# Kernel tuning notes

Measured on AMD Instinct MI355X. Metric: run time of the kernel, lower is better.

The kernel has to match this reference:

```python
import jax, jax.numpy as jnp
import numpy as np

B = 16      # graphs
NPG = 1024  # nodes per graph (equal-sized, contiguous)
N = B * NPG
K = 12      # knn neighbors
DM = 128    # d_model
DH = 256    # d_hidden = 2*d_model
L = 3       # num_layers
DI = 2 * DM + 4  # msg mlp input dim


def _mlp2(x, W1, b1, W2, b2):
    return jax.nn.silu(x @ W1 + b1) @ W2 + b2


def setup_inputs() -> dict:
    key = jax.random.key(0)
    ks = list(jax.random.split(key, 16))
    def nrm(k, shape, fan):
        return jax.random.normal(k, shape, jnp.float32) / np.float32(np.sqrt(fan))
    return dict(
        x=jax.random.normal(ks[0], (N, 3), jnp.float32),
        batch=(jnp.arange(N) // NPG).astype(jnp.int32),
        in_W1=nrm(ks[1], (3, DM), 3), in_b1=jnp.zeros((DM,), jnp.float32),
        in_W2=nrm(ks[2], (DM, DM), DM), in_b2=jnp.zeros((DM,), jnp.float32),
        msg_W1=nrm(ks[3], (L, DI, DH), DI), msg_b1=jnp.zeros((L, DH), jnp.float32),
        msg_W2=nrm(ks[4], (L, DH, DM), DH), msg_b2=jnp.zeros((L, DM), jnp.float32),
        upd_W1=nrm(ks[5], (L, 2 * DM, DH), 2 * DM), upd_b1=jnp.zeros((L, DH), jnp.float32),
        upd_W2=nrm(ks[6], (L, DH, DM), DH), upd_b2=jnp.zeros((L, DM), jnp.float32),
        norm_w=jnp.ones((L, DM), jnp.float32), norm_b=jnp.zeros((L, DM), jnp.float32),
        norm_ms=jnp.ones((L, DM), jnp.float32),
        gate_W1=nrm(ks[7], (DM, DM), DM), gate_b1=jnp.zeros((DM,), jnp.float32),
        gate_W2=nrm(ks[8], (DM, 1), DM), gate_b2=jnp.zeros((1,), jnp.float32),
        head_W1=nrm(ks[9], (DM, DM), DM), head_b1=jnp.zeros((DM,), jnp.float32),
        head_W2=nrm(ks[10], (DM, 1), DM), head_b2=jnp.zeros((1,), jnp.float32),
    )


def _knn_edges(pos):
    # pos: [N,2]; graphs are contiguous blocks of NPG nodes -> blocked knn
    p3 = pos.reshape(B, NPG, 2)
    d2 = jnp.sum((p3[:, :, None, :] - p3[:, None, :, :]) ** 2, axis=-1)  # [B,n,n]
    d2 = jnp.where(jnp.eye(NPG, dtype=bool)[None], jnp.inf, d2)          # no self loops
    idx = jax.lax.top_k(-d2, K)[1]  # [B,n,K] nearest neighbors (sources)
    offs = (jnp.arange(B) * NPG)[:, None, None]
    src = (idx + offs).reshape(-1)
    dst = jnp.broadcast_to(jnp.arange(N).reshape(B, NPG, 1), (B, NPG, K)).reshape(-1)
    return src, dst


def _graph_norm(h, batch, cnt, w, b, ms):
    # PyG GraphNorm: out = w * (h - ms*mean) / sqrt(var + eps) + b, per-graph stats
    mean = jax.ops.segment_sum(h, batch, B) / cnt
    out = h - mean[batch] * ms
    var = jax.ops.segment_sum(out ** 2, batch, B) / cnt
    return w * out / jnp.sqrt(var + 1e-5)[batch] + b


def _forward(x, batch, in_W1, in_b1, in_W2, in_b2, msg_W1, msg_b1, msg_W2, msg_b2,
             upd_W1, upd_b1, upd_W2, upd_b2, norm_w, norm_b, norm_ms,
             gate_W1, gate_b1, gate_W2, gate_b2, head_W1, head_b1, head_W2, head_b2):
    pos = x[:, 1:3]
    src, dst = _knn_edges(pos)
    # edge_attr = [dx, dy, dist, ds]
    dp = pos[src] - pos[dst]
    dist = jnp.sqrt(jnp.sum(dp ** 2, axis=-1, keepdims=True) + 1e-12)
    ds = x[src, 0:1] - x[dst, 0:1]
    ea = jnp.concatenate([dp, dist, ds], axis=-1)  # [E,4]

    h = _mlp2(x, in_W1, in_b1, in_W2, in_b2)       # [N,DM]
    cnt = jax.ops.segment_sum(jnp.ones((N,), h.dtype), batch, B)[:, None]

    for i in range(L):
        m_in = jnp.concatenate([h[dst], h[src], ea], axis=-1)       # [E,2*DM+4]
        m = _mlp2(m_in, msg_W1[i], msg_b1[i], msg_W2[i], msg_b2[i])  # [E,DM]
        agg = jax.ops.segment_sum(m, dst, N)                         # scatter_add
        dh = _mlp2(jnp.concatenate([h, agg], axis=-1),
                   upd_W1[i], upd_b1[i], upd_W2[i], upd_b2[i])
        h = h + dh  # dropout is identity at inference
        h = _graph_norm(h, batch, cnt, norm_w[i], norm_b[i], norm_ms[i])

    # gated attention pool: segment softmax over gate logits
    gl = (jnp.tanh(h @ gate_W1 + gate_b1) @ gate_W2 + gate_b2)[:, 0]  # [N]
    gmax = jax.ops.segment_max(gl, batch, B)
    e = jnp.exp(gl - gmax[batch])
    a = e / jax.ops.segment_sum(e, batch, B)[batch]
    pooled = jax.ops.segment_sum(h * a[:, None], batch, B)            # [B,DM]

    return _mlp2(pooled, head_W1, head_b1, head_W2, head_b2)[:, 0]    # [B]


def reference(x, batch, in_W1, in_b1, in_W2, in_b2, msg_W1, msg_b1, msg_W2, msg_b2,
              upd_W1, upd_b1, upd_W2, upd_b2, norm_w, norm_b, norm_ms,
              gate_W1, gate_b1, gate_W2, gate_b2, head_W1, head_b1, head_W2, head_b2):
    return _forward(x, batch, in_W1, in_b1, in_W2, in_b2, msg_W1, msg_b1, msg_W2, msg_b2,
                    upd_W1, upd_b1, upd_W2, upd_b2, norm_w, norm_b, norm_ms,
                    gate_W1, gate_b1, gate_W2, gate_b2, head_W1, head_b1, head_W2, head_b2)
```

## Files before the change

kernel.cpp:

```cpp
#include <hip/hip_runtime.h>
#include <math.h>

#define NPTS 16384
#define BGR 16
#define NPGR 1024
#define KNN 12
#define DM 128
#define DH 256
#define NL 3
#define EDG (NPTS*KNN)

typedef unsigned short u16;
typedef unsigned int u32;
typedef __attribute__((ext_vector_type(8))) short short8;
typedef __attribute__((ext_vector_type(4))) float floatx4;

__device__ __forceinline__ float silu_f(float x) {
    return x / (1.0f + __expf(-x));
}
__device__ __forceinline__ u16 f2bf(float f) {
    union { float f; u32 u; } v; v.f = f;
    u32 r = v.u + 0x7fffu + ((v.u >> 16) & 1u);
    return (u16)(r >> 16);
}
__device__ __forceinline__ float bf2f(u16 b) {
    union { u32 u; float f; } v; v.u = ((u32)b) << 16;
    return v.f;
}

#define KPPB 16
#define PSTR 209
__global__ __launch_bounds__(256) void knn_kernel(const float* __restrict__ x,
                                                  int* __restrict__ srcb,
                                                  float* __restrict__ ea) {
#pragma clang fp contract(off)
    __shared__ float px[NPGR], py[NPGR], s0[NPGR];
    __shared__ float sdf[KPPB * PSTR];
    __shared__ int   sif[KPPB * PSTR];
    __shared__ int   sel[KPPB][KNN];
    int t = threadIdx.x;
    int g   = blockIdx.x / (NPGR / KPPB);
    int blk = blockIdx.x % (NPGR / KPPB);
    int base = g * NPGR;
    for (int j = t; j < NPGR; j += 256) {
        const float* xp = x + (size_t)(base + j) * 3;
        s0[j] = xp[0]; px[j] = xp[1]; py[j] = xp[2];
    }
    __syncthreads();
    int r  = t & 15;
    int pt = t >> 4;
    int il = blk * KPPB + pt;
    float xi = px[il], yi = py[il];
    float nd[KNN]; int ni[KNN];
#pragma unroll
    for (int k = 0; k < KNN; ++k) { nd[k] = 3.4e38f; ni[k] = 0x7fffffff; }
    int j0 = r * 64;
    for (int jj = 0; jj < 64; ++jj) {
        int j = j0 + jj;
        if (j == il) continue;
        float dx = px[j] - xi;
        float dy = py[j] - yi;
        float dx2 = dx * dx;
        float dy2 = dy * dy;
        float d2 = dx2 + dy2;
        if (d2 < nd[KNN-1]) {
            float cd = d2; int ci = j;
#pragma unroll
            for (int k = 0; k < KNN; ++k) {
                bool sw = cd < nd[k];
                float tdv = sw ? nd[k] : cd;
                nd[k] = sw ? cd : nd[k];
                cd = tdv;
                int tiv = sw ? ni[k] : ci;
                ni[k] = sw ? ci : ni[k];
                ci = tiv;
            }
        }
    }
#pragma unroll
    for (int k = 0; k < KNN; ++k) {
        sdf[pt * PSTR + r * 13 + k] = nd[k];
        sif[pt * PSTR + r * 13 + k] = ni[k];
    }
    __syncthreads();
    if (r == 0) {
        int head[16];
#pragma unroll
        for (int q = 0; q < 16; ++q) head[q] = 0;
#pragma unroll
        for (int k = 0; k < KNN; ++k) {
            float bd = 3.4e38f; int bi = 0x7fffffff; int bq = 0;
#pragma unroll
            for (int q = 0; q < 16; ++q) {
                int hq = head[q];
                float d = (hq < KNN) ? sdf[pt * PSTR + q * 13 + hq] : 3.4e38f;
                int  ix = (hq < KNN) ? sif[pt * PSTR + q * 13 + hq] : 0x7fffffff;
                if (d < bd || (d == bd && ix < bi)) { bd = d; bi = ix; bq = q; }
            }
            head[bq]++;
            sel[pt][k] = bi;
        }
    }
    __syncthreads();
    if (r < KNN) {
        int k = r;
        int j = sel[pt][k];
        size_t e = (size_t)(base + il) * KNN + k;
        srcb[e] = base + j;
        float x0i = s0[il];
        float dpx = px[j] - xi, dpy = py[j] - yi;
        float a = dpx * dpx;
        float b = dpy * dpy;
        float dist = sqrtf(a + b + 1e-12f);
        float dsv = s0[j] - x0i;
        *(float4*)(ea + e * 4) = make_float4(dpx, dpy, dist, dsv);
    }
}

__global__ __launch_bounds__(128) void in_mlp_kernel(const float* __restrict__ x,
    const float* __restrict__ W1, const float* __restrict__ b1,
    const float* __restrict__ W2, const float* __restrict__ b2,
    float* __restrict__ h) {
    __shared__ float hid[8][DM];
    __shared__ float xl[8][3];
    int t = threadIdx.x;
    int nb = blockIdx.x * 8;
    if (t < 24) xl[t / 3][t % 3] = x[(size_t)nb * 3 + t];
    __syncthreads();
    float w0 = W1[t], w1 = W1[DM + t], w2 = W1[2 * DM + t], bb = b1[t];
#pragma unroll
    for (int gi = 0; gi < 8; ++gi) {
        float v = xl[gi][0] * w0 + xl[gi][1] * w1 + xl[gi][2] * w2 + bb;
        hid[gi][t] = silu_f(v);
    }
    __syncthreads();
    float acc[8];
    float b2v = b2[t];
#pragma unroll
    for (int gi = 0; gi < 8; ++gi) acc[gi] = b2v;
    for (int k = 0; k < DM; ++k) {
        float w = W2[k * DM + t];
#pragma unroll
        for (int gi = 0; gi < 8; ++gi) acc[gi] += hid[gi][k] * w;
    }
#pragma unroll
    for (int gi = 0; gi < 8; ++gi) h[(size_t)(nb + gi) * DM + t] = acc[gi];
}

#define MBM 64
#define MBN 128
#define MBK 32
#define MLDA 40

__global__ __launch_bounds__(256) void mgemm_kernel(
    const float* __restrict__ A0, int k0, int lda0,
    const float* __restrict__ A1, int lda1,
    const u16* __restrict__ Wh, const u16* __restrict__ Wl, int K,
    const float* __restrict__ bias, int biasN,
    const float* __restrict__ resid, int ldres,
    float* __restrict__ out, int ldout,
    int act)
{
    __shared__ __align__(16) u16 Ash[MBM * MLDA];
    __shared__ __align__(16) u16 Asl[MBM * MLDA];
    __shared__ __align__(16) u16 Bsh[MBN * MLDA];
    __shared__ __align__(16) u16 Bsl[MBN * MLDA];
    int t = threadIdx.x;
    int row0 = blockIdx.x * MBM, col0 = blockIdx.y * MBN;
    int lane = t & 63, w = t >> 6;
    int wm = (w >> 1) * 32, wn = (w & 1) * 64;
    int quad = lane >> 4, r15 = lane & 15;
    int arow = t >> 2, acol = (t & 3) * 8;
    int brow = t >> 1, bcol = (t & 1) * 16;

    floatx4 acc[2][4];
#pragma unroll
    for (int m = 0; m < 2; ++m)
#pragma unroll
        for (int n = 0; n < 4; ++n) acc[m][n] = (floatx4){0.f, 0.f, 0.f, 0.f};

    for (int kt = 0; kt < K; kt += MBK) {
        const float* Ap = (kt < k0)
            ? (A0 + (size_t)(row0 + arow) * lda0 + kt + acol)
            : (A1 + (size_t)(row0 + arow) * lda1 + (kt - k0) + acol);
        float4 a0 = ((const float4*)Ap)[0];
        float4 a1 = ((const float4*)Ap)[1];
        const u16* Bph = Wh + (size_t)(col0 + brow) * K + kt + bcol;
        const u16* Bpl = Wl + (size_t)(col0 + brow) * K + kt + bcol;
        uint4 bh0 = ((const uint4*)Bph)[0];
        uint4 bh1 = ((const uint4*)Bph)[1];
        uint4 bl0 = ((const uint4*)Bpl)[0];
        uint4 bl1 = ((const uint4*)Bpl)[1];
        __syncthreads();
        float av[8] = {a0.x,a0.y,a0.z,a0.w, a1.x,a1.y,a1.z,a1.w};
        u32 uh[4], ul[4];
#pragma unroll
        for (int i = 0; i < 4; ++i) {
            u16 h0 = f2bf(av[2*i]);
            u16 h1 = f2bf(av[2*i+1]);
            u16 l0 = f2bf(av[2*i]   - bf2f(h0));
            u16 l1 = f2bf(av[2*i+1] - bf2f(h1));
            uh[i] = (u32)h0 | ((u32)h1 << 16);
            ul[i] = (u32)l0 | ((u32)l1 << 16);
        }
        *(uint4*)(Ash + arow * MLDA + acol) = make_uint4(uh[0],uh[1],uh[2],uh[3]);
        *(uint4*)(Asl + arow * MLDA + acol) = make_uint4(ul[0],ul[1],ul[2],ul[3]);
        uint4* bdh = (uint4*)(Bsh + brow * MLDA + bcol);
        uint4* bdl = (uint4*)(Bsl + brow * MLDA + bcol);
        bdh[0] = bh0; bdh[1] = bh1;
        bdl[0] = bl0; bdl[1] = bl1;
        __syncthreads();
        short8 ah[2], alo[2], bhf[4], blf[4];
#pragma unroll
        for (int m = 0; m < 2; ++m) {
            ah[m]  = *(const short8*)(Ash + (wm + m*16 + r15) * MLDA + quad*8);
            alo[m] = *(const short8*)(Asl + (wm + m*16 + r15) * MLDA + quad*8);
        }
#pragma unroll
        for (int n = 0; n < 4; ++n) {
            bhf[n] = *(const short8*)(Bsh + (wn + n*16 + r15) * MLDA + quad*8);
            blf[n] = *(const short8*)(Bsl + (wn + n*16 + r15) * MLDA + quad*8);
        }
#pragma unroll
        for (int m = 0; m < 2; ++m)
#pragma unroll
            for (int n = 0; n < 4; ++n) {
                acc[m][n] = __builtin_amdgcn_mfma_f32_16x16x32_bf16(ah[m],  bhf[n], acc[m][n], 0, 0, 0);
                acc[m][n] = __builtin_amdgcn_mfma_f32_16x16x32_bf16(ah[m],  blf[n], acc[m][n], 0, 0, 0);
                acc[m][n] = __builtin_amdgcn_mfma_f32_16x16x32_bf16(alo[m], bhf[n], acc[m][n], 0, 0, 0);
            }
    }
#pragma unroll
    for (int n = 0; n < 4; ++n) {
        int col = col0 + wn + n*16 + r15;
        float bv = (bias && col < biasN) ? bias[col] : 0.f;
#pragma unroll
        for (int m = 0; m < 2; ++m) {
#pragma unroll
            for (int reg = 0; reg < 4; ++reg) {
                int row = row0 + wm + m*16 + quad*4 + reg;
                float v = acc[m][n][reg] + bv;
                if (act == 1) v = silu_f(v);
                else if (act == 2) v = tanhf(v);
                if (resid) v += resid[(size_t)row * ldres + col];
                out[(size_t)row * ldout + col] = v;
            }
        }
    }
}

__global__ __launch_bounds__(256) void edge_agg_kernel(
    const float* __restrict__ CS,
    const int* __restrict__ srcb, const float* __restrict__ ea,
    const float* __restrict__ W1ea,
    float* __restrict__ HS)
{
    int i = blockIdx.x, t = threadIdx.x;
    __shared__ int ss[KNN];
    __shared__ float sea[KNN * 4];
    if (t < KNN) ss[t] = srcb[(size_t)i * KNN + t];
    if (t < KNN * 4) sea[t] = ea[(size_t)i * KNN * 4 + t];
    __syncthreads();
    float base = CS[(size_t)i * 512 + t];
    float wa = W1ea[t], wb = W1ea[DH + t], wc = W1ea[2 * DH + t], wd = W1ea[3 * DH + t];
    float hs = 0.f;
#pragma unroll
    for (int e = 0; e < KNN; ++e) {
        float v = base + CS[(size_t)ss[e] * 512 + 256 + t]
                + sea[e * 4 + 0] * wa + sea[e * 4 + 1] * wb
                + sea[e * 4 + 2] * wc + sea[e * 4 + 3] * wd;
        hs += silu_f(v);
    }
    HS[(size_t)i * DH + t] = hs;
}

__global__ __launch_bounds__(256) void norm_part_kernel(const float* __restrict__ hn,
                                                        float* __restrict__ psum)
{
    int g = blockIdx.x, blk = blockIdx.y;
    int t = threadIdx.x, d = t & 127, half = t >> 7;
    size_t base = ((size_t)g * NPGR + (size_t)blk * 128 + half * 64) * DM;
    float s = 0.f, s2 = 0.f;
    for (int n = 0; n < 64; ++n) {
        float v = hn[base + (size_t)n * DM + d];
        s += v; s2 += v * v;
    }
    __shared__ float ps[2][DM], ps2[2][DM];
    ps[half][d] = s; ps2[half][d] = s2;
    __syncthreads();
    if (t < DM) {
        psum[(((size_t)g * 8 + blk) * 2 + 0) * DM + d] = ps[0][d] + ps[1][d];
        psum[(((size_t)g * 8 + blk) * 2 + 1) * DM + d] = ps2[0][d] + ps2[1][d];
    }
}

__global__ __launch_bounds__(256) void norm_apply_kernel(const float* __restrict__ hn,
    float* __restrict__ h, const float* __restrict__ psum,
    const float* __restrict__ w, const float* __restrict__ b, const float* __restrict__ ms)
{
    int g = blockIdx.x, blk = blockIdx.y, t = threadIdx.x;
    __shared__ float mmv[DM], rst[DM], wv[DM], bv[DM];
    if (t < DM) {
        float sum = 0.f, sq = 0.f;
        for (int q = 0; q < 8; ++q) {
            sum += psum[(((size_t)g * 8 + q) * 2 + 0) * DM + t];
            sq  += psum[(((size_t)g * 8 + q) * 2 + 1) * DM + t];
        }
        float mean = sum * (1.0f / NPGR);
        float mm = mean * ms[t];
        float var = sq * (1.0f / NPGR) - 2.f * mm * mean + mm * mm;
        mmv[t] = mm;
        rst[t] = 1.0f / sqrtf(var + 1e-5f);
        wv[t] = w[t]; bv[t] = b[t];
    }
    __syncthreads();
    size_t base = ((size_t)g * NPGR + (size_t)blk * 128) * DM;
    for (int i = t; i < 128 * DM; i += 256) {
        int dd = i & 127;
        float v = hn[base + i];
        h[base + i] = wv[dd] * (v - mmv[dd]) * rst[dd] + bv[dd];
    }
}

__global__ __launch_bounds__(256) void gate_dot_kernel(const float* __restrict__ Gh,
    const float* __restrict__ gW2, const float* __restrict__ gb2,
    float* __restrict__ gl)
{
    int t = threadIdx.x, lane = t & 63, w = t >> 6;
    int node = blockIdx.x * 4 + w;
    const float* gp = Gh + (size_t)node * DM;
    float v = gp[lane] * gW2[lane] + gp[lane + 64] * gW2[lane + 64];
    for (int off = 32; off > 0; off >>= 1) v += __shfl_down(v, off, 64);
    if (lane == 0) gl[node] = v + gb2[0];
}

__global__ __launch_bounds__(256) void pool_stats_kernel(const float* __restrict__ gl,
                                                         float* __restrict__ gstat)
{
    int g = blockIdx.x, t = threadIdx.x, lane = t & 63, w = t >> 6;
    __shared__ float red[4];
    const float* gp = gl + (size_t)g * NPGR;
    float mx = -3.4e38f;
    for (int n = t; n < NPGR; n += 256) mx = fmaxf(mx, gp[n]);
    for (int off = 32; off > 0; off >>= 1) mx = fmaxf(mx, __shfl_down(mx, off, 64));
    if (lane == 0) red[w] = mx;
    __syncthreads();
    float gmax = fmaxf(fmaxf(red[0], red[1]), fmaxf(red[2], red[3]));
    __syncthreads();
    float se = 0.f;
    for (int n = t; n < NPGR; n += 256) se += __expf(gp[n] - gmax);
    for (int off = 32; off > 0; off >>= 1) se += __shfl_down(se, off, 64);
    if (lane == 0) red[w] = se;
    __syncthreads();
    if (t == 0) { gstat[g * 2] = gmax; gstat[g * 2 + 1] = red[0] + red[1] + red[2] + red[3]; }
}

__global__ __launch_bounds__(256) void pool_part_kernel(const float* __restrict__ h,
    const float* __restrict__ gl, const float* __restrict__ gstat,
    float* __restrict__ ppool)
{
    int g = blockIdx.x, blk = blockIdx.y;
    int t = threadIdx.x, d = t & 127, half = t >> 7;
    float gmax = gstat[g * 2];
    size_t nbase = (size_t)g * NPGR + (size_t)blk * 128 + half * 64;
    float p = 0.f;
    for (int n = 0; n < 64; ++n)
        p += __expf(gl[nbase + n] - gmax) * h[(nbase + n) * DM + d];
    __shared__ float ps[2][DM];
    ps[half][d] = p;
    __syncthreads();
    if (t < DM) ppool[((size_t)g * 8 + blk) * DM + d] = ps[0][d] + ps[1][d];
}

__global__ __launch_bounds__(128) void pool_head_kernel(const float* __restrict__ ppool,
    const float* __restrict__ gstat,
    const float* __restrict__ hW1, const float* __restrict__ hb1,
    const float* __restrict__ hW2, const float* __restrict__ hb2,
    float* __restrict__ outp)
{
    int g = blockIdx.x, t = threadIdx.x;
    __shared__ float pl[DM];
    __shared__ float red[2];
    float ssum = gstat[g * 2 + 1];
    float p = 0.f;
    for (int q = 0; q < 8; ++q) p += ppool[((size_t)g * 8 + q) * DM + t];
    pl[t] = p / ssum;
    __syncthreads();
    float a = hb1[t];
    for (int k = 0; k < DM; ++k) a += pl[k] * hW1[k * DM + t];
    a = silu_f(a);
    float vv = a * hW2[t];
    int lane = t & 63, w = t >> 6;
    for (int off = 32; off > 0; off >>= 1) vv += __shfl_down(vv, off, 64);
    if (lane == 0) red[w] = vv;
    __syncthreads();
    if (t == 0) outp[g] = red[0] + red[1] + hb2[0];
}

__global__ __launch_bounds__(256) void precompute_kernel(
    const float* __restrict__ msgW2, const float* __restrict__ msgb2,
    const float* __restrict__ updW1, const float* __restrict__ updb1,
    float* __restrict__ W2U, float* __restrict__ bias2)
{
    int bid = blockIdx.x; int t = threadIdx.x;
    if (bid < NL * DH) {
        int l = bid / DH, k = bid % DH;
        const float* w2row = msgW2 + (size_t)l * DH * DM + (size_t)k * DM;
        const float* u1 = updW1 + (size_t)l * 2 * DM * DH;
        float acc = 0.f;
        for (int j = 0; j < DM; ++j) acc += w2row[j] * u1[(size_t)(DM + j) * DH + t];
        W2U[(size_t)l * DH * DH + (size_t)k * DH + t] = acc;
    } else {
        int l = bid - NL * DH;
        const float* u1 = updW1 + (size_t)l * 2 * DM * DH;
        const float* b2 = msgb2 + (size_t)l * DM;
        float acc = updb1[(size_t)l * DH + t];
        for (int j = 0; j < DM; ++j) acc += 12.0f * b2[j] * u1[(size_t)(DM + j) * DH + t];
        bias2[(size_t)l * DH + t] = acc;
    }
}

struct WJob { const float* src; u16* dh; u16* dl; int K, N, ldd, off; };
struct WJobs { WJob j[16]; };
__global__ __launch_bounds__(256) void wprep_kernel(WJobs jobs) {
    WJob jb = jobs.j[blockIdx.y];
    int n = blockIdx.x;
    if (n >= jb.N) return;
    for (int k = threadIdx.x; k < jb.K; k += 256) {
        float v = jb.src[(size_t)k * jb.N + n];
        u16 hi = f2bf(v);
        u16 lo = f2bf(v - bf2f(hi));
        jb.dh[(size_t)n * jb.ldd + jb.off + k] = hi;
        jb.dl[(size_t)n * jb.ldd + jb.off + k] = lo;
    }
}

extern "C" void kernel_launch(void* const* d_in, const int* in_sizes, int n_in,
                              void* d_out, int out_size, void* d_ws, size_t ws_size,
                              hipStream_t stream) {
    const float* x     = (const float*)d_in[0];
    const float* inW1  = (const float*)d_in[2];
    const float* inb1  = (const float*)d_in[3];
    const float* inW2  = (const float*)d_in[4];
    const float* inb2  = (const float*)d_in[5];
    const float* msgW1 = (const float*)d_in[6];
    const float* msgb1 = (const float*)d_in[7];
    const float* msgW2 = (const float*)d_in[8];
    const float* msgb2 = (const float*)d_in[9];
    const float* updW1 = (const float*)d_in[10];
    const float* updb1 = (const float*)d_in[11];
    const float* updW2 = (const float*)d_in[12];
    const float* updb2 = (const float*)d_in[13];
    const float* nw    = (const float*)d_in[14];
    const float* nb    = (const float*)d_in[15];
    const float* nms   = (const float*)d_in[16];
    const float* gW1   = (const float*)d_in[17];
    const float* gb1   = (const float*)d_in[18];
    const float* gW2   = (const float*)d_in[19];
    const float* gb2   = (const float*)d_in[20];
    const float* hW1   = (const float*)d_in[21];
    const float* hb1   = (const float*)d_in[22];
    const float* hW2   = (const float*)d_in[23];
    const float* hb2   = (const float*)d_in[24];
    float* outp = (float*)d_out;

    float* ws    = (float*)d_ws;
    float* h     = ws;
    float* CSb   = h + (size_t)NPTS * DM;
    float* HSb   = CSb + (size_t)NPTS * 512;
    float* W2U   = HSb + (size_t)NPTS * DH;
    float* bias2 = W2U + (size_t)NL * DH * DH;
    float* glb   = bias2 + NL * DH;
    int*   srcb  = (int*)(glb + NPTS);
    float* eab   = (float*)(srcb + EDG);
    float* psum  = eab + (size_t)EDG * 4;
    float* gstat = psum + 16 * 8 * 2 * DM;
    float* ppool = gstat + 32;
    u16* wsp = (u16*)(ppool + 16 * 8 * DM);
    u16* WCSh = wsp;                                 u16* WCSl = WCSh + (size_t)NL * 512 * DM;
    u16* WTh = WCSl + (size_t)NL * 512 * DM;         u16* WTl = WTh + (size_t)NL * DH * 384;
    u16* WUh = WTl + (size_t)NL * DH * 384;          u16* WUl = WUh + (size_t)NL * DM * DH;
    u16* WGh = WUl + (size_t)NL * DM * DH;           u16* WGl = WGh + (size_t)DM * DM;

    hipLaunchKernelGGL(precompute_kernel, dim3(NL * DH + NL), dim3(DH), 0, stream,
                       msgW2, msgb2, updW1, updb1, W2U, bias2);

    WJobs jobs;
    int ji = 0;
    for (int l = 0; l < NL; ++l) {
        jobs.j[ji++] = WJob{ msgW1 + (size_t)l * 260 * DH,            WCSh + (size_t)l * 512 * DM,            WCSl + (size_t)l * 512 * DM,            128, 256, 128, 0 };
        jobs.j[ji++] = WJob{ msgW1 + (size_t)l * 260 * DH + 128 * DH, WCSh + (size_t)l * 512 * DM + 256 * DM, WCSl + (size_t)l * 512 * DM + 256 * DM, 128, 256, 128, 0 };
        jobs.j[ji++] = WJob{ updW1 + (size_t)l * 256 * DH,            WTh + (size_t)l * DH * 384, WTl + (size_t)l * DH * 384, 128, 256, 384, 0 };
        jobs.j[ji++] = WJob{ W2U   + (size_t)l * DH * DH,             WTh + (size_t)l * DH * 384, WTl + (size_t)l * DH * 384, 256, 256, 384, 128 };
        jobs.j[ji++] = WJob{ updW2 + (size_t)l * DH * DM,             WUh + (size_t)l * DM * DH, WUl + (size_t)l * DM * DH, 256, 128, 256, 0 };
    }
    jobs.j[ji++] = WJob{ gW1, WGh, WGl, 128, 128, 128, 0 };
    hipLaunchKernelGGL(wprep_kernel, dim3(256, 16), dim3(256), 0, stream, jobs);

    hipLaunchKernelGGL(knn_kernel, dim3(NPTS / KPPB), dim3(256), 0, stream, x, srcb, eab);
    hipLaunchKernelGGL(in_mlp_kernel, dim3(NPTS / 8), dim3(128), 0, stream,
                       x, inW1, inb1, inW2, inb2, h);

    for (int l = 0; l < NL; ++l) {
        const float* W1l = msgW1 + (size_t)l * 260 * DH;
        hipLaunchKernelGGL(mgemm_kernel, dim3(NPTS / MBM, 512 / MBN), dim3(256), 0, stream,
            h, DM, DM, (const float*)nullptr, 0,
            WCSh + (size_t)l * 512 * DM, WCSl + (size_t)l * 512 * DM, DM,
            msgb1 + (size_t)l * DH, 256, (const float*)nullptr, 0, CSb, 512, 0);
        hipLaunchKernelGGL(edge_agg_kernel, dim3(NPTS), dim3(DH), 0, stream,
            CSb, srcb, eab, W1l + (size_t)2 * DM * DH, HSb);
        hipLaunchKernelGGL(mgemm_kernel, dim3(NPTS / MBM, DH / MBN), dim3(256), 0, stream,
            h, DM, DM, HSb, DH,
            WTh + (size_t)l * DH * 384, WTl + (size_t)l * DH * 384, 384,
            bias2 + (size_t)l * DH, DH, (const float*)nullptr, 0, CSb, 512, 1);
        hipLaunchKernelGGL(mgemm_kernel, dim3(NPTS / MBM, DM / MBN), dim3(256), 0, stream,
            CSb, 512, 512, (const float*)nullptr, 0,
            WUh + (size_t)l * DM * DH, WUl + (size_t)l * DM * DH, DH,
            updb2 + (size_t)l * DM, DM, h, DM, HSb, DM, 0);
        hipLaunchKernelGGL(norm_part_kernel, dim3(BGR, 8), dim3(256), 0, stream, HSb, psum);
        hipLaunchKernelGGL(norm_apply_kernel, dim3(BGR, 8), dim3(256), 0, stream,
            HSb, h, psum, nw + (size_t)l * DM, nb + (size_t)l * DM, nms + (size_t)l * DM);
    }

    hipLaunchKernelGGL(mgemm_kernel, dim3(NPTS / MBM, DM / MBN), dim3(256), 0, stream,
        h, DM, DM, (const float*)nullptr, 0,
        WGh, WGl, DM, gb1, DM, (const float*)nullptr, 0, CSb, DM, 2);
    hipLaunchKernelGGL(gate_dot_kernel, dim3(NPTS / 4), dim3(256), 0, stream,
        CSb, gW2, gb2, glb);

    hipLaunchKernelGGL(pool_stats_kernel, dim3(BGR), dim3(256), 0, stream, glb, gstat);
    hipLaunchKernelGGL(pool_part_kernel, dim3(BGR, 8), dim3(256), 0, stream, h, glb, gstat, ppool);
    hipLaunchKernelGGL(pool_head_kernel, dim3(BGR), dim3(128), 0, stream,
        ppool, gstat, hW1, hb1, hW2, hb2, outp);
}
```

Baseline: 541.7 us.

## Store GEMM activations pre-split into bf16 hi/lo pairs by producers

Producers (in_mlp, edge_agg, norm_apply, the silu GEMM epilogue) now write activations as bf16 hi/lo split arrays, so the GEMM A-tile load becomes a direct copy instead of per-tile float-to-bf16 splitting. The same split work is no longer repeated by every column block of each GEMM, and the bytes read for A stay equal. The kNN kernel also switches to interleaved float2 positions, a per-lane rotated scan order that spreads LDS bank accesses, and an index tie-break for equal distances. The cost is extra writes and workspace for the split buffers, plus slightly more compare work in the kNN insertion.

```diff
diff --git a/kernel.cpp b/kernel.cpp
--- a/kernel.cpp
+++ b/kernel.cpp
@@ -34,7 +34,8 @@
                                                   int* __restrict__ srcb,
                                                   float* __restrict__ ea) {
 #pragma clang fp contract(off)
-    __shared__ float px[NPGR], py[NPGR], s0[NPGR];
+    __shared__ float2 pxy[NPGR];
+    __shared__ float s0[NPGR];
     __shared__ float sdf[KPPB * PSTR];
     __shared__ int   sif[KPPB * PSTR];
     __shared__ int   sel[KPPB][KNN];
@@ -44,30 +45,33 @@
     int base = g * NPGR;
     for (int j = t; j < NPGR; j += 256) {
         const float* xp = x + (size_t)(base + j) * 3;
-        s0[j] = xp[0]; px[j] = xp[1]; py[j] = xp[2];
+        s0[j] = xp[0];
+        pxy[j] = make_float2(xp[1], xp[2]);
     }
     __syncthreads();
     int r  = t & 15;
     int pt = t >> 4;
     int il = blk * KPPB + pt;
-    float xi = px[il], yi = py[il];
+    float2 pil = pxy[il];
+    float xi = pil.x, yi = pil.y;
     float nd[KNN]; int ni[KNN];
 #pragma unroll
     for (int k = 0; k < KNN; ++k) { nd[k] = 3.4e38f; ni[k] = 0x7fffffff; }
     int j0 = r * 64;
     for (int jj = 0; jj < 64; ++jj) {
-        int j = j0 + jj;
+        int j = j0 + ((jj + r) & 63);
         if (j == il) continue;
-        float dx = px[j] - xi;
-        float dy = py[j] - yi;
+        float2 p = pxy[j];
+        float dx = p.x - xi;
+        float dy = p.y - yi;
         float dx2 = dx * dx;
         float dy2 = dy * dy;
         float d2 = dx2 + dy2;
-        if (d2 < nd[KNN-1]) {
+        if (d2 < nd[KNN-1] || (d2 == nd[KNN-1] && j < ni[KNN-1])) {
             float cd = d2; int ci = j;
 #pragma unroll
             for (int k = 0; k < KNN; ++k) {
-                bool sw = cd < nd[k];
+                bool sw = (cd < nd[k]) || (cd == nd[k] && ci < ni[k]);
                 float tdv = sw ? nd[k] : cd;
                 nd[k] = sw ? cd : nd[k];
                 cd = tdv;
@@ -108,7 +112,8 @@
         size_t e = (size_t)(base + il) * KNN + k;
         srcb[e] = base + j;
         float x0i = s0[il];
-        float dpx = px[j] - xi, dpy = py[j] - yi;
+        float2 pj = pxy[j];
+        float dpx = pj.x - xi, dpy = pj.y - yi;
         float a = dpx * dpx;
         float b = dpy * dpy;
         float dist = sqrtf(a + b + 1e-12f);
@@ -120,7 +125,7 @@
 __global__ __launch_bounds__(128) void in_mlp_kernel(const float* __restrict__ x,
     const float* __restrict__ W1, const float* __restrict__ b1,
     const float* __restrict__ W2, const float* __restrict__ b2,
-    float* __restrict__ h) {
+    float* __restrict__ h, u16* __restrict__ hh, u16* __restrict__ hl) {
     __shared__ float hid[8][DM];
     __shared__ float xl[8][3];
     int t = threadIdx.x;
@@ -144,7 +149,14 @@
         for (int gi = 0; gi < 8; ++gi) acc[gi] += hid[gi][k] * w;
     }
 #pragma unroll
-    for (int gi = 0; gi < 8; ++gi) h[(size_t)(nb + gi) * DM + t] = acc[gi];
+    for (int gi = 0; gi < 8; ++gi) {
+        size_t idx = (size_t)(nb + gi) * DM + t;
+        float v = acc[gi];
+        h[idx] = v;
+        u16 hi = f2bf(v);
+        hh[idx] = hi;
+        hl[idx] = f2bf(v - bf2f(hi));
+    }
 }
 
 #define MBM 64
@@ -153,12 +165,12 @@
 #define MLDA 40
 
 __global__ __launch_bounds__(256) void mgemm_kernel(
-    const float* __restrict__ A0, int k0, int lda0,
-    const float* __restrict__ A1, int lda1,
+    const u16* __restrict__ A0h, const u16* __restrict__ A0l, int k0, int lda0,
+    const u16* __restrict__ A1h, const u16* __restrict__ A1l, int lda1,
     const u16* __restrict__ Wh, const u16* __restrict__ Wl, int K,
     const float* __restrict__ bias, int biasN,
     const float* __restrict__ resid, int ldres,
-    float* __restrict__ out, int ldout,
+    float* __restrict__ outf, u16* __restrict__ outh, u16* __restrict__ outl, int ldout,
     int act)
 {
     __shared__ __align__(16) u16 Ash[MBM * MLDA];
@@ -180,11 +192,16 @@
         for (int n = 0; n < 4; ++n) acc[m][n] = (floatx4){0.f, 0.f, 0.f, 0.f};
 
     for (int kt = 0; kt < K; kt += MBK) {
-        const float* Ap = (kt < k0)
-            ? (A0 + (size_t)(row0 + arow) * lda0 + kt + acol)
-            : (A1 + (size_t)(row0 + arow) * lda1 + (kt - k0) + acol);
-        float4 a0 = ((const float4*)Ap)[0];
-        float4 a1 = ((const float4*)Ap)[1];
+        const u16 *Aph, *Apl;
+        if (kt < k0) {
+            Aph = A0h + (size_t)(row0 + arow) * lda0 + kt + acol;
+            Apl = A0l + (size_t)(row0 + arow) * lda0 + kt + acol;
+        } else {
+            Aph = A1h + (size_t)(row0 + arow) * lda1 + (kt - k0) + acol;
+            Apl = A1l + (size_t)(row0 + arow) * lda1 + (kt - k0) + acol;
+        }
+        uint4 avh = *(const uint4*)Aph;
+        uint4 avl = *(const uint4*)Apl;
         const u16* Bph = Wh + (size_t)(col0 + brow) * K + kt + bcol;
         const u16* Bpl = Wl + (size_t)(col0 + brow) * K + kt + bcol;
         uint4 bh0 = ((const uint4*)Bph)[0];
@@ -192,19 +209,8 @@
         uint4 bl0 = ((const uint4*)Bpl)[0];
         uint4 bl1 = ((const uint4*)Bpl)[1];
         __syncthreads();
-        float av[8] = {a0.x,a0.y,a0.z,a0.w, a1.x,a1.y,a1.z,a1.w};
-        u32 uh[4], ul[4];
-#pragma unroll
-        for (int i = 0; i < 4; ++i) {
-            u16 h0 = f2bf(av[2*i]);
-            u16 h1 = f2bf(av[2*i+1]);
-            u16 l0 = f2bf(av[2*i]   - bf2f(h0));
-            u16 l1 = f2bf(av[2*i+1] - bf2f(h1));
-            uh[i] = (u32)h0 | ((u32)h1 << 16);
-            ul[i] = (u32)l0 | ((u32)l1 << 16);
-        }
-        *(uint4*)(Ash + arow * MLDA + acol) = make_uint4(uh[0],uh[1],uh[2],uh[3]);
-        *(uint4*)(Asl + arow * MLDA + acol) = make_uint4(ul[0],ul[1],ul[2],ul[3]);
+        *(uint4*)(Ash + arow * MLDA + acol) = avh;
+        *(uint4*)(Asl + arow * MLDA + acol) = avl;
         uint4* bdh = (uint4*)(Bsh + brow * MLDA + bcol);
         uint4* bdl = (uint4*)(Bsl + brow * MLDA + bcol);
         bdh[0] = bh0; bdh[1] = bh1;
@@ -243,7 +249,13 @@
                 if (act == 1) v = silu_f(v);
                 else if (act == 2) v = tanhf(v);
                 if (resid) v += resid[(size_t)row * ldres + col];
-                out[(size_t)row * ldout + col] = v;
+                size_t oidx = (size_t)row * ldout + col;
+                if (outf) outf[oidx] = v;
+                if (outh) {
+                    u16 hi = f2bf(v);
+                    outh[oidx] = hi;
+                    outl[oidx] = f2bf(v - bf2f(hi));
+                }
             }
         }
     }
@@ -253,7 +265,7 @@
     const float* __restrict__ CS,
     const int* __restrict__ srcb, const float* __restrict__ ea,
     const float* __restrict__ W1ea,
-    float* __restrict__ HS)
+    u16* __restrict__ HSh, u16* __restrict__ HSl)
 {
     int i = blockIdx.x, t = threadIdx.x;
     __shared__ int ss[KNN];
@@ -271,7 +283,10 @@
                 + sea[e * 4 + 2] * wc + sea[e * 4 + 3] * wd;
         hs += silu_f(v);
     }
-    HS[(size_t)i * DH + t] = hs;
+    size_t oidx = (size_t)i * DH + t;
+    u16 hi = f2bf(hs);
+    HSh[oidx] = hi;
+    HSl[oidx] = f2bf(hs - bf2f(hi));
 }
 
 __global__ __launch_bounds__(256) void norm_part_kernel(const float* __restrict__ hn,
@@ -295,7 +310,8 @@
 }
 
 __global__ __launch_bounds__(256) void norm_apply_kernel(const float* __restrict__ hn,
-    float* __restrict__ h, const float* __restrict__ psum,
+    float* __restrict__ h, u16* __restrict__ hh, u16* __restrict__ hl,
+    const float* __restrict__ psum,
     const float* __restrict__ w, const float* __restrict__ b, const float* __restrict__ ms)
 {
     int g = blockIdx.x, blk = blockIdx.y, t = threadIdx.x;
@@ -318,7 +334,11 @@
     for (int i = t; i < 128 * DM; i += 256) {
         int dd = i & 127;
         float v = hn[base + i];
-        h[base + i] = wv[dd] * (v - mmv[dd]) * rst[dd] + bv[dd];
+        float o = wv[dd] * (v - mmv[dd]) * rst[dd] + bv[dd];
+        h[base + i] = o;
+        u16 hi = f2bf(o);
+        hh[base + i] = hi;
+        hl[base + i] = f2bf(o - bf2f(hi));
     }
 }
 
@@ -467,8 +487,8 @@
     float* ws    = (float*)d_ws;
     float* h     = ws;
     float* CSb   = h + (size_t)NPTS * DM;
-    float* HSb   = CSb + (size_t)NPTS * 512;
-    float* W2U   = HSb + (size_t)NPTS * DH;
+    float* hnb   = CSb + (size_t)NPTS * 512;
+    float* W2U   = hnb + (size_t)NPTS * DM;
     float* bias2 = W2U + (size_t)NL * DH * DH;
     float* glb   = bias2 + NL * DH;
     int*   srcb  = (int*)(glb + NPTS);
@@ -476,8 +496,13 @@
     float* psum  = eab + (size_t)EDG * 4;
     float* gstat = psum + 16 * 8 * 2 * DM;
     float* ppool = gstat + 32;
-    u16* wsp = (u16*)(ppool + 16 * 8 * DM);
-    u16* WCSh = wsp;                                 u16* WCSl = WCSh + (size_t)NL * 512 * DM;
+    u16* hh  = (u16*)(ppool + 16 * 8 * DM);
+    u16* hl  = hh + (size_t)NPTS * DM;
+    u16* HSh = hl + (size_t)NPTS * DM;
+    u16* HSl = HSh + (size_t)NPTS * DH;
+    u16* Th  = HSl + (size_t)NPTS * DH;
+    u16* Tl  = Th + (size_t)NPTS * DH;
+    u16* WCSh = Tl + (size_t)NPTS * DH;              u16* WCSl = WCSh + (size_t)NL * 512 * DM;
     u16* WTh = WCSl + (size_t)NL * 512 * DM;         u16* WTl = WTh + (size_t)NL * DH * 384;
     u16* WUh = WTl + (size_t)NL * DH * 384;          u16* WUl = WUh + (size_t)NL * DM * DH;
     u16* WGh = WUl + (size_t)NL * DM * DH;           u16* WGl = WGh + (size_t)DM * DM;
@@ -499,34 +524,38 @@
 
     hipLaunchKernelGGL(knn_kernel, dim3(NPTS / KPPB), dim3(256), 0, stream, x, srcb, eab);
     hipLaunchKernelGGL(in_mlp_kernel, dim3(NPTS / 8), dim3(128), 0, stream,
-                       x, inW1, inb1, inW2, inb2, h);
+                       x, inW1, inb1, inW2, inb2, h, hh, hl);
 
     for (int l = 0; l < NL; ++l) {
         const float* W1l = msgW1 + (size_t)l * 260 * DH;
         hipLaunchKernelGGL(mgemm_kernel, dim3(NPTS / MBM, 512 / MBN), dim3(256), 0, stream,
-            h, DM, DM, (const float*)nullptr, 0,
+            hh, hl, DM, DM, (const u16*)nullptr, (const u16*)nullptr, 0,
             WCSh + (size_t)l * 512 * DM, WCSl + (size_t)l * 512 * DM, DM,
-            msgb1 + (size_t)l * DH, 256, (const float*)nullptr, 0, CSb, 512, 0);
+            msgb1 + (size_t)l * DH, 256, (const float*)nullptr, 0,
+            CSb, (u16*)nullptr, (u16*)nullptr, 512, 0);
         hipLaunchKernelGGL(edge_agg_kernel, dim3(NPTS), dim3(DH), 0, stream,
-            CSb, srcb, eab, W1l + (size_t)2 * DM * DH, HSb);
+            CSb, srcb, eab, W1l + (size_t)2 * DM * DH, HSh, HSl);
         hipLaunchKernelGGL(mgemm_kernel, dim3(NPTS / MBM, DH / MBN), dim3(256), 0, stream,
-            h, DM, DM, HSb, DH,
+            hh, hl, DM, DM, HSh, HSl, DH,
             WTh + (size_t)l * DH * 384, WTl + (size_t)l * DH * 384, 384,
-            bias2 + (size_t)l * DH, DH, (const float*)nullptr, 0, CSb, 512, 1);
+            bias2 + (size_t)l * DH, DH, (const float*)nullptr, 0,
+            (float*)nullptr, Th, Tl, DH, 1);
         hipLaunchKernelGGL(mgemm_kernel, dim3(NPTS / MBM, DM / MBN), dim3(256), 0, stream,
-            CSb, 512, 512, (const float*)nullptr, 0,
+            Th, Tl, DH, DH, (const u16*)nullptr, (const u16*)nullptr, 0,
             WUh + (size_t)l * DM * DH, WUl + (size_t)l * DM * DH, DH,
-            updb2 + (size_t)l * DM, DM, h, DM, HSb, DM, 0);
-        hipLaunchKernelGGL(norm_part_kernel, dim3(BGR, 8), dim3(256), 0, stream, HSb, psum);
+            updb2 + (size_t)l * DM, DM, h, DM,
+            hnb, (u16*)nullptr, (u16*)nullptr, DM, 0);
+        hipLaunchKernelGGL(norm_part_kernel, dim3(BGR, 8), dim3(256), 0, stream, hnb, psum);
         hipLaunchKernelGGL(norm_apply_kernel, dim3(BGR, 8), dim3(256), 0, stream,
-            HSb, h, psum, nw + (size_t)l * DM, nb + (size_t)l * DM, nms + (size_t)l * DM);
+            hnb, h, hh, hl, psum, nw + (size_t)l * DM, nb + (size_t)l * DM, nms + (size_t)l * DM);
     }
 
     hipLaunchKernelGGL(mgemm_kernel, dim3(NPTS / MBM, DM / MBN), dim3(256), 0, stream,
-        h, DM, DM, (const float*)nullptr, 0,
-        WGh, WGl, DM, gb1, DM, (const float*)nullptr, 0, CSb, DM, 2);
+        hh, hl, DM, DM, (const u16*)nullptr, (const u16*)nullptr, 0,
+        WGh, WGl, DM, gb1, DM, (const float*)nullptr, 0,
+        hnb, (u16*)nullptr, (u16*)nullptr, DM, 2);
     hipLaunchKernelGGL(gate_dot_kernel, dim3(NPTS / 4), dim3(256), 0, stream,
-        CSb, gW2, gb2, glb);
+        hnb, gW2, gb2, glb);
 
     hipLaunchKernelGGL(pool_stats_kernel, dim3(BGR), dim3(256), 0, stream, glb, gstat);
     hipLaunchKernelGGL(pool_part_kernel, dim3(BGR, 8), dim3(256), 0, stream, h, glb, gstat, ppool);
```

After: 595.3 us. 1.1x slower.
